# Performance work log

Hardware: AMD Instinct MI355X
Metric: run time of the kernel (lower is better)

Reference implementation:

```python
import jax, jax.numpy as jnp
import numpy as np

MUL = 128                 # multiplicity per irrep (in == out)
IR_DIMS = (1, 3, 5)       # 2l+1 for 0e, 1o, 2e
FEAT = MUL * sum(IR_DIMS) # 1152
N = 100000
ALPHA = 1.0 / np.sqrt(np.float32(MUL))  # e3nn element path normalization, single path per output irrep


def setup_inputs() -> dict:
    key = jax.random.key(0)
    k_x, k0, k1, k2 = jax.random.split(key, 4)
    x = jax.random.normal(k_x, (N, FEAT), dtype=jnp.float32)
    w0 = jax.random.normal(k0, (MUL, MUL), dtype=jnp.float32)
    w1 = jax.random.normal(k1, (MUL, MUL), dtype=jnp.float32)
    w2 = jax.random.normal(k2, (MUL, MUL), dtype=jnp.float32)
    return {"x": x, "w0": w0, "w1": w1, "w2": w2}


def reference(x, w0, w1, w2):
    # Block-diagonal equivariant linear: for each irrep block, mix the
    # multiplicity axis u->w, leaving the (2l+1) component axis i intact.
    ws = (w0, w1, w2)
    outs = []
    off = 0
    for w, d in zip(ws, IR_DIMS):
        blk = d * MUL
        chunk = x[:, off:off + blk].reshape(-1, MUL, d)   # [N, u, i]
        y = jnp.einsum('nui,uw->nwi', chunk, w) * ALPHA    # [N, w, i]
        outs.append(y.reshape(-1, blk))
        off += blk
    return jnp.concatenate(outs, axis=-1)  # [N, FEAT]
```

## Files before the change

kernel.cpp:

```cpp
#include <hip/hip_runtime.h>


typedef __attribute__((ext_vector_type(8))) short short8;
typedef __attribute__((ext_vector_type(4))) float floatx4;

#define ALPHA 0.08838834764831845f
#define FEAT 1152

__device__ inline unsigned short bf16_rne(float f) {
    unsigned int u = __float_as_uint(f);
    unsigned int r = u + 0x7fffu + ((u >> 16) & 1u);
    return (unsigned short)(r >> 16);
}

template <int D, int OFF, int MINBPC>
__launch_bounds__(256, MINBPC)
__global__ void eq_linear_kernel(const float* __restrict__ x,
                                 const float* __restrict__ wmat,
                                 float* __restrict__ out, int n) {
    constexpr int C   = 128 * D;
    constexpr int C4  = C / 4;
    constexpr int R   = 16;
    constexpr int AP  = 136;
    constexpr int APL = R * AP + 8;
    constexpr int OP  = C + 4;

    __shared__ unsigned short xs[D * APL];
    __shared__ float os[(D == 1) ? 1 : (R * OP)];

    const int tid  = threadIdx.x;
    const int lane = tid & 63;
    const int wave = tid >> 6;
    const int l16  = lane & 15;
    const int quad = lane >> 4;
    const int rowbase = blockIdx.x * R;

    constexpr int ITERS = (R * C4) / 256;
#pragma unroll
    for (int it = 0; it < ITERS; ++it) {
        int idx = tid + it * 256;
        int r  = idx / C4;
        int c4 = idx - r * C4;
        float4 v = make_float4(0.f, 0.f, 0.f, 0.f);
        if (rowbase + r < n) {
            v = *(reinterpret_cast<const float4*>(
                  x + (size_t)(rowbase + r) * FEAT + OFF) + c4);
        }
        if (D == 1) {
            unsigned int p0 = (unsigned int)bf16_rne(v.x) | ((unsigned int)bf16_rne(v.y) << 16);
            unsigned int p1 = (unsigned int)bf16_rne(v.z) | ((unsigned int)bf16_rne(v.w) << 16);
            unsigned int* lp = reinterpret_cast<unsigned int*>(&xs[r * AP + c4 * 4]);
            lp[0] = p0;
            lp[1] = p1;
        } else {
            float vv[4] = {v.x, v.y, v.z, v.w};
#pragma unroll
            for (int j = 0; j < 4; ++j) {
                int c = 4 * c4 + j;
                int u = c / D;
                int i = c - u * D;
                xs[i * APL + r * AP + u] = bf16_rne(vv[j]);
            }
        }
    }

    short8 bfrag[2][4];
#pragma unroll
    for (int ntl = 0; ntl < 2; ++ntl) {
        int wcol = (wave * 2 + ntl) * 16 + l16;
#pragma unroll
        for (int k = 0; k < 4; ++k) {
            int u0 = k * 32 + quad * 8;
            short8 f;
#pragma unroll
            for (int j = 0; j < 8; ++j) {
                f[j] = (short)bf16_rne(wmat[(u0 + j) * 128 + wcol]);
            }
            bfrag[ntl][k] = f;
        }
    }

    __syncthreads();

#pragma unroll
    for (int i = 0; i < D; ++i) {
        floatx4 acc[2] = {floatx4{0, 0, 0, 0}, floatx4{0, 0, 0, 0}};
#pragma unroll
        for (int k = 0; k < 4; ++k) {
            const short8 a = *reinterpret_cast<const short8*>(
                &xs[i * APL + l16 * AP + k * 32 + quad * 8]);
            acc[0] = __builtin_amdgcn_mfma_f32_16x16x32_bf16(a, bfrag[0][k], acc[0], 0, 0, 0);
            acc[1] = __builtin_amdgcn_mfma_f32_16x16x32_bf16(a, bfrag[1][k], acc[1], 0, 0, 0);
        }
        if (D == 1) {
#pragma unroll
            for (int ntl = 0; ntl < 2; ++ntl) {
                int col = OFF + (wave * 2 + ntl) * 16 + l16;
#pragma unroll
                for (int r = 0; r < 4; ++r) {
                    int row = rowbase + quad * 4 + r;
                    if (row < n) out[(size_t)row * FEAT + col] = acc[ntl][r] * ALPHA;
                }
            }
        } else {
#pragma unroll
            for (int ntl = 0; ntl < 2; ++ntl) {
                int wc = (wave * 2 + ntl) * 16 + l16;
#pragma unroll
                for (int r = 0; r < 4; ++r) {
                    os[(quad * 4 + r) * OP + wc * D + i] = acc[ntl][r] * ALPHA;
                }
            }
        }
    }

    if (D > 1) {
        __syncthreads();
#pragma unroll
        for (int it = 0; it < ITERS; ++it) {
            int idx = tid + it * 256;
            int r  = idx / C4;
            int c4 = idx - r * C4;
            if (rowbase + r < n) {
                float4 v = *reinterpret_cast<const float4*>(&os[r * OP + 4 * c4]);
                *(reinterpret_cast<float4*>(
                      out + (size_t)(rowbase + r) * FEAT + OFF) + c4) = v;
            }
        }
    }
}

extern "C" void kernel_launch(void* const* d_in, const int* in_sizes, int n_in,
                              void* d_out, int out_size, void* d_ws, size_t ws_size,
                              hipStream_t stream) {
    const float* x  = (const float*)d_in[0];
    const float* w0 = (const float*)d_in[1];
    const float* w1 = (const float*)d_in[2];
    const float* w2 = (const float*)d_in[3];
    float* out = (float*)d_out;

    int n = in_sizes[0] / FEAT;
    int grid = (n + 15) / 16;
    dim3 blk(256);

    eq_linear_kernel<1, 0, 4>  <<<grid, blk, 0, stream>>>(x, w0, out, n);
    eq_linear_kernel<3, 128, 4><<<grid, blk, 0, stream>>>(x, w1, out, n);
    eq_linear_kernel<5, 512, 2><<<grid, blk, 0, stream>>>(x, w2, out, n);
}
```

Before: 842.6 us.

## Register-stage x loads and write outputs directly, dropping LDS output staging

All global loads of x are issued into registers before the weight fragments are loaded. The bf16 conversion and LDS stores now happen after that, so the load latency overlaps with the weight setup. The output staging buffer in shared memory and its second barrier are removed. Each lane keeps accumulators for all D components and writes D contiguous floats per row straight to global memory. The D=5 kernel now uses the same launch bound of 4 blocks per CU, which trades register pressure for occupancy. Direct writes of 12 or 20 bytes per lane at a D-float stride may coalesce less well than the float4 stores did before.

```diff
diff --git a/kernel.cpp b/kernel.cpp
--- a/kernel.cpp
+++ b/kernel.cpp
@@ -13,8 +13,8 @@
     return (unsigned short)(r >> 16);
 }
 
-template <int D, int OFF, int MINBPC>
-__launch_bounds__(256, MINBPC)
+template <int D, int OFF>
+__launch_bounds__(256, 4)
 __global__ void eq_linear_kernel(const float* __restrict__ x,
                                  const float* __restrict__ wmat,
                                  float* __restrict__ out, int n) {
@@ -23,10 +23,8 @@
     constexpr int R   = 16;
     constexpr int AP  = 136;
     constexpr int APL = R * AP + 8;
-    constexpr int OP  = C + 4;
 
     __shared__ unsigned short xs[D * APL];
-    __shared__ float os[(D == 1) ? 1 : (R * OP)];
 
     const int tid  = threadIdx.x;
     const int lane = tid & 63;
@@ -36,31 +34,16 @@
     const int rowbase = blockIdx.x * R;
 
     constexpr int ITERS = (R * C4) / 256;
+    floatx4 xv[ITERS];
 #pragma unroll
     for (int it = 0; it < ITERS; ++it) {
         int idx = tid + it * 256;
         int r  = idx / C4;
         int c4 = idx - r * C4;
-        float4 v = make_float4(0.f, 0.f, 0.f, 0.f);
+        xv[it] = floatx4{0.f, 0.f, 0.f, 0.f};
         if (rowbase + r < n) {
-            v = *(reinterpret_cast<const float4*>(
-                  x + (size_t)(rowbase + r) * FEAT + OFF) + c4);
-        }
-        if (D == 1) {
-            unsigned int p0 = (unsigned int)bf16_rne(v.x) | ((unsigned int)bf16_rne(v.y) << 16);
-            unsigned int p1 = (unsigned int)bf16_rne(v.z) | ((unsigned int)bf16_rne(v.w) << 16);
-            unsigned int* lp = reinterpret_cast<unsigned int*>(&xs[r * AP + c4 * 4]);
-            lp[0] = p0;
-            lp[1] = p1;
-        } else {
-            float vv[4] = {v.x, v.y, v.z, v.w};
-#pragma unroll
-            for (int j = 0; j < 4; ++j) {
-                int c = 4 * c4 + j;
-                int u = c / D;
-                int i = c - u * D;
-                xs[i * APL + r * AP + u] = bf16_rne(vv[j]);
-            }
+            xv[it] = *(reinterpret_cast<const floatx4*>(
+                       x + (size_t)(rowbase + r) * FEAT + OFF) + c4);
         }
     }
 
@@ -80,51 +63,61 @@
         }
     }
 
+#pragma unroll
+    for (int it = 0; it < ITERS; ++it) {
+        int idx = tid + it * 256;
+        int r  = idx / C4;
+        int c4 = idx - r * C4;
+        floatx4 v = xv[it];
+        if (D == 1) {
+            unsigned int p0 = (unsigned int)bf16_rne(v.x) | ((unsigned int)bf16_rne(v.y) << 16);
+            unsigned int p1 = (unsigned int)bf16_rne(v.z) | ((unsigned int)bf16_rne(v.w) << 16);
+            unsigned int* lp = reinterpret_cast<unsigned int*>(&xs[r * AP + c4 * 4]);
+            lp[0] = p0;
+            lp[1] = p1;
+        } else {
+#pragma unroll
+            for (int j = 0; j < 4; ++j) {
+                int c = 4 * c4 + j;
+                int u = c / D;
+                int i = c - u * D;
+                xs[i * APL + r * AP + u] = bf16_rne(v[j]);
+            }
+        }
+    }
+
     __syncthreads();
+
+    floatx4 acc[2][D];
+#pragma unroll
+    for (int ntl = 0; ntl < 2; ++ntl)
+#pragma unroll
+        for (int i = 0; i < D; ++i)
+            acc[ntl][i] = floatx4{0.f, 0.f, 0.f, 0.f};
 
 #pragma unroll
     for (int i = 0; i < D; ++i) {
-        floatx4 acc[2] = {floatx4{0, 0, 0, 0}, floatx4{0, 0, 0, 0}};
 #pragma unroll
         for (int k = 0; k < 4; ++k) {
             const short8 a = *reinterpret_cast<const short8*>(
                 &xs[i * APL + l16 * AP + k * 32 + quad * 8]);
-            acc[0] = __builtin_amdgcn_mfma_f32_16x16x32_bf16(a, bfrag[0][k], acc[0], 0, 0, 0);
-            acc[1] = __builtin_amdgcn_mfma_f32_16x16x32_bf16(a, bfrag[1][k], acc[1], 0, 0, 0);
-        }
-        if (D == 1) {
-#pragma unroll
-            for (int ntl = 0; ntl < 2; ++ntl) {
-                int col = OFF + (wave * 2 + ntl) * 16 + l16;
-#pragma unroll
-                for (int r = 0; r < 4; ++r) {
-                    int row = rowbase + quad * 4 + r;
-                    if (row < n) out[(size_t)row * FEAT + col] = acc[ntl][r] * ALPHA;
-                }
-            }
-        } else {
-#pragma unroll
-            for (int ntl = 0; ntl < 2; ++ntl) {
-                int wc = (wave * 2 + ntl) * 16 + l16;
-#pragma unroll
-                for (int r = 0; r < 4; ++r) {
-                    os[(quad * 4 + r) * OP + wc * D + i] = acc[ntl][r] * ALPHA;
-                }
-            }
+            acc[0][i] = __builtin_amdgcn_mfma_f32_16x16x32_bf16(a, bfrag[0][k], acc[0][i], 0, 0, 0);
+            acc[1][i] = __builtin_amdgcn_mfma_f32_16x16x32_bf16(a, bfrag[1][k], acc[1][i], 0, 0, 0);
         }
     }
 
-    if (D > 1) {
-        __syncthreads();
 #pragma unroll
-        for (int it = 0; it < ITERS; ++it) {
-            int idx = tid + it * 256;
-            int r  = idx / C4;
-            int c4 = idx - r * C4;
-            if (rowbase + r < n) {
-                float4 v = *reinterpret_cast<const float4*>(&os[r * OP + 4 * c4]);
-                *(reinterpret_cast<float4*>(
-                      out + (size_t)(rowbase + r) * FEAT + OFF) + c4) = v;
+    for (int ntl = 0; ntl < 2; ++ntl) {
+        const int wc = (wave * 2 + ntl) * 16 + l16;
+#pragma unroll
+        for (int r = 0; r < 4; ++r) {
+            const int row = rowbase + quad * 4 + r;
+            if (row < n) {
+                float* p = out + (size_t)row * FEAT + OFF + wc * D;
+                float s[D];
+#pragma unroll
+                for (int i = 0; i < D; ++i) s[i] = acc[ntl][i][r] * ALPHA;
+                __builtin_memcpy(p, s, sizeof(s));
             }
         }
     }
@@ -143,7 +136,7 @@
     int grid = (n + 15) / 16;
     dim3 blk(256);
 
-    eq_linear_kernel<1, 0, 4>  <<<grid, blk, 0, stream>>>(x, w0, out, n);
-    eq_linear_kernel<3, 128, 4><<<grid, blk, 0, stream>>>(x, w1, out, n);
-    eq_linear_kernel<5, 512, 2><<<grid, blk, 0, stream>>>(x, w2, out, n);
+    eq_linear_kernel<1, 0>  <<<grid, blk, 0, stream>>>(x, w0, out, n);
+    eq_linear_kernel<3, 128><<<grid, blk, 0, stream>>>(x, w1, out, n);
+    eq_linear_kernel<5, 512><<<grid, blk, 0, stream>>>(x, w2, out, n);
 }
```

Result: faster. 805.1 us (-4.5%).
